# Performance work log

Hardware: AMD Instinct MI355X
Metric: run time of the kernel (lower is better)

Reference implementation:

```python
import jax, jax.numpy as jnp
import numpy as np


def setup_inputs() -> dict:
    key = jax.random.key(0)
    B, S, D = 64, 1024, 1024
    ks = jax.random.split(key, 13)
    bound = 1.0 / np.sqrt(D)
    u = lambda k, shape: jax.random.uniform(k, shape, jnp.float32, -bound, bound)
    inp = {
        "emb": jax.random.normal(ks[0], (B, S, D), jnp.float32),
        "W_ii": u(ks[1], (D, D)), "b_ii": u(ks[2], (D,)),
        "W_if": u(ks[3], (D, D)), "b_if": u(ks[4], (D,)),
        "W_ig": u(ks[5], (D, D)), "b_ig": u(ks[6], (D,)),
        "W_io": u(ks[7], (D, D)), "b_io": u(ks[8], (D,)),
        "W_hi": u(ks[9], (D, D)),
        "W_hf": u(ks[10], (D, D)),
        "W_hg": u(ks[11], (D, D)),
        "W_ho": u(ks[12], (D, D)),
    }
    return inp


def _lstm_forward(emb, W_ii, b_ii, W_if, b_if, W_ig, b_ig, W_io, b_io,
                  W_hi, W_hf, W_hg, W_ho):
    B, S, D = emb.shape
    # Precompute all input projections in one batched GEMM: [B,S,4D]
    Wx = jnp.concatenate([W_ii, W_if, W_ig, W_io], axis=0)      # [4D, D]
    bx = jnp.concatenate([b_ii, b_if, b_ig, b_io], axis=0)      # [4D]
    x_proj = jnp.einsum('bsd,ed->bse', emb, Wx) + bx            # [B,S,4D]
    x_proj = jnp.swapaxes(x_proj, 0, 1)                         # [S,B,4D]
    # Fuse the 4 hidden matmuls into one [D,4D] weight
    Wh = jnp.concatenate([W_hi, W_hf, W_hg, W_ho], axis=0)      # [4D, D]

    h0 = jnp.zeros((B, D), emb.dtype)
    c0 = jnp.zeros((B, D), emb.dtype)

    def step(carry, xp_t):
        h, c = carry
        gates = xp_t + h @ Wh.T                                 # [B,4D]
        xi, xf, xg, xo = jnp.split(gates, 4, axis=-1)
        i_t = jax.nn.sigmoid(xi)
        f_t = jax.nn.sigmoid(xf)
        g_t = jnp.tanh(xg)
        o_t = jax.nn.sigmoid(xo)
        c = f_t * c + i_t * g_t
        h = o_t * jnp.tanh(c)
        return (h, c), None

    (h, c), _ = jax.lax.scan(step, (h0, c0), x_proj)
    return h


def reference(emb, W_ii, b_ii, W_if, b_if, W_ig, b_ig, W_io, b_io,
              W_hi, W_hf, W_hg, W_ho):
    return _lstm_forward(emb, W_ii, b_ii, W_if, b_if, W_ig, b_ig,
                         W_io, b_io, W_hi, W_hf, W_hg, W_ho)
```

## Files before the change

### kernel.cpp

```cpp
#include <hip/hip_runtime.h>
#include <stdint.h>

#define NB 64
#define NS 1024
#define ND 1024
#define NG 4096
#define CHUNK 128
#define NCHUNK 8
#define RING 32

typedef __attribute__((ext_vector_type(4))) float f32x4;
typedef __attribute__((ext_vector_type(8))) short bf16x8;

__device__ __forceinline__ float bf2f(uint16_t u) {
  return __uint_as_float(((uint32_t)u) << 16);
}
__device__ __forceinline__ uint16_t f2bf(float f) {
  uint32_t x = __float_as_uint(f);
  return (uint16_t)((x + 0x7fffu + ((x >> 16) & 1u)) >> 16);
}
__device__ __forceinline__ float sigmoidf_(float x) {
  return 1.f / (1.f + __expf(-x));
}
__device__ __forceinline__ float tanhf_(float x) {
  return 1.f - 2.f / (__expf(x + x) + 1.f);
}
__device__ __forceinline__ void gload_lds16(const void* g, void* l) {
  __builtin_amdgcn_global_load_lds(
      (const __attribute__((address_space(1))) uint32_t*)g,
      (__attribute__((address_space(3))) uint32_t*)l, 16, 0, 0);
}
__device__ __forceinline__ void gload_lds16_nc(const void* g, void* l) {
  __builtin_amdgcn_global_load_lds(
      (const __attribute__((address_space(1))) uint32_t*)g,
      (__attribute__((address_space(3))) uint32_t*)l, 16, 0, 17);
}

__global__ void k_cvt(const float* __restrict__ src, uint16_t* __restrict__ dst, int n4) {
  int stride = gridDim.x * blockDim.x;
  for (int i = blockIdx.x * blockDim.x + threadIdx.x; i < n4; i += stride) {
    float4 v = ((const float4*)src)[i];
    ushort4 o;
    o.x = f2bf(v.x); o.y = f2bf(v.y); o.z = f2bf(v.z); o.w = f2bf(v.w);
    ((ushort4*)dst)[i] = o;
  }
}

__device__ __forceinline__ void gemm_tile(const uint16_t* __restrict__ A0,
                                          const uint16_t* __restrict__ Wx,
                                          uint16_t* __restrict__ XP,
                                          int b, int nb, int tid, char* lmem) {
  uint16_t* lAx = (uint16_t*)lmem;
  uint16_t* lBx = (uint16_t*)(lmem + 8192);
  const uint16_t* B0 = Wx + (size_t)(nb * 128) * ND;
  const int lane = tid & 63, wv = tid >> 6;
  const int m_off = (wv >> 1) << 6, n_off = (wv & 1) << 6;

  f32x4 acc[4][4] = {};
  for (int kb = 0; kb < ND / 32; ++kb) {
    const int k0 = kb * 32;
#pragma unroll
    for (int j = 0; j < 2; ++j) {
      int cid = j * 256 + tid;
      int row = cid >> 2, cc = cid & 3;
      int cs = cc ^ (row & 3);
      gload_lds16(A0 + (size_t)row * ND + k0 + cs * 8, (char*)lAx + cid * 16);
      gload_lds16(B0 + (size_t)row * ND + k0 + cs * 8, (char*)lBx + cid * 16);
    }
    __syncthreads();
    bf16x8 af[4], bfr[4];
#pragma unroll
    for (int i = 0; i < 4; ++i) {
      int row = m_off + i * 16 + (lane & 15);
      int ch = (lane >> 4) ^ (row & 3);
      af[i] = *(const bf16x8*)((const char*)lAx + row * 64 + ch * 16);
      int rowb = n_off + i * 16 + (lane & 15);
      int chb = (lane >> 4) ^ (rowb & 3);
      bfr[i] = *(const bf16x8*)((const char*)lBx + rowb * 64 + chb * 16);
    }
#pragma unroll
    for (int i = 0; i < 4; ++i)
#pragma unroll
      for (int j2 = 0; j2 < 4; ++j2)
        acc[i][j2] = __builtin_amdgcn_mfma_f32_16x16x32_bf16(af[i], bfr[j2], acc[i][j2], 0, 0, 0);
    __syncthreads();
  }
#pragma unroll
  for (int i = 0; i < 4; ++i)
#pragma unroll
    for (int j2 = 0; j2 < 4; ++j2)
#pragma unroll
      for (int r = 0; r < 4; ++r) {
        int m = m_off + i * 16 + ((lane >> 4) << 2) + r;
        int n = nb * 128 + n_off + j2 * 16 + (lane & 15);
        XP[((size_t)(m * NB + b)) * NG + n] = f2bf(acc[i][j2][r]);
      }
}

__global__ __launch_bounds__(512, 2) void k_fused(
    const uint16_t* __restrict__ embb,
    const uint16_t* __restrict__ Wx,
    const uint16_t* __restrict__ Wh,
    uint16_t* __restrict__ xpA, uint16_t* __restrict__ xpB,
    const float* __restrict__ b_i, const float* __restrict__ b_f,
    const float* __restrict__ b_g, const float* __restrict__ b_o,
    uint16_t* __restrict__ hring,
    float* __restrict__ cbuf,
    uint32_t* __restrict__ flags,
    float* __restrict__ out, int chunk) {
  extern __shared__ char smem[];
  const int bid = blockIdx.x;
  const int tid = threadIdx.x;

  if (chunk < 0 || bid >= 128) {
    const int gc = (chunk < 0) ? 0 : chunk + 1;
    if (gc >= NCHUNK) return;
    uint16_t* XP = (gc & 1) ? xpB : xpA;
    const int nw = (chunk < 0) ? 512 : 256;
    const int widx = ((chunk < 0) ? bid : bid - 128) * 2 + (tid >> 8);
    const int t256 = tid & 255;
    char* lmem = smem + ((tid >> 8) << 14);
    const int t0g = gc * CHUNK;
    for (int job = widx; job < 64 * 32; job += nw) {
      int b = job & 63, nb = job >> 6;
      gemm_tile(embb + ((size_t)b * NS + t0g) * ND, Wx, XP, b, nb, t256, lmem);
    }
    return;
  }

  uint16_t* lH = (uint16_t*)smem;
  int* lds_sync = (int*)(smem + 32768);
  const int t0 = chunk * CHUNK;
  const uint16_t* XP = (chunk & 1) ? xpB : xpA;

  const int lane = tid & 63, wv = tid >> 6;
  const int xcd = bid & 7;
  const int g_b = xcd >> 1;
  const int g_d = (xcd & 1) + ((bid >> 3) << 1);

  const int q = lane >> 4, nl = lane & 15;
  const int g = nl & 3;
  const int d_loc = wv * 4 + (nl >> 2);
  const int dg = g_d * 32 + d_loc;
  const int bg0 = g_b * 16 + q * 4;

  const uint16_t* wrow = Wh + ((size_t)g * ND + dg) * ND;
  bf16x8 wfr[32];
#pragma unroll
  for (int kk = 0; kk < 32; ++kk)
    wfr[kk] = *(const bf16x8*)(wrow + kk * 32 + q * 8);

  const float* bptr = (g == 0) ? b_i : (g == 1) ? b_f : (g == 2) ? b_g : b_o;
  const float Bv = bptr[dg];

  float c0, c1, c2, c3;
  if (t0 == 0) {
    c0 = c1 = c2 = c3 = 0.f;
  } else {
    c0 = cbuf[(size_t)(bg0 + 0) * ND + dg];
    c1 = cbuf[(size_t)(bg0 + 1) * ND + dg];
    c2 = cbuf[(size_t)(bg0 + 2) * ND + dg];
    c3 = cbuf[(size_t)(bg0 + 3) * ND + dg];
  }

  if (tid == 0)
    __hip_atomic_store(lds_sync, t0, __ATOMIC_RELAXED, __HIP_MEMORY_SCOPE_WORKGROUP);
  __syncthreads();

  const uint16_t* xp0 = XP + ((size_t)bg0) * NG + ((size_t)g << 10) + dg;
  uint16_t xc0 = xp0[0], xc1 = xp0[NG], xc2 = xp0[2 * (size_t)NG], xc3 = xp0[3 * (size_t)NG];

#pragma unroll 1
  for (int t = t0; t < t0 + CHUNK; ++t) {
    f32x4 a0 = {0,0,0,0}, a1 = {0,0,0,0}, a2 = {0,0,0,0}, a3 = {0,0,0,0};
    if (t > 0) {
      if (wv == 0) {
        const uint32_t* fl = flags + ((((size_t)(t - 1) * 4 + g_b) << 5) + (lane & 31)) * 4;
        uint32_t v;
        do {
          v = __hip_atomic_load(fl, __ATOMIC_RELAXED, __HIP_MEMORY_SCOPE_AGENT);
        } while (__any(v == 0));
        if (lane == 0)
          __hip_atomic_store(lds_sync, t, __ATOMIC_RELAXED, __HIP_MEMORY_SCOPE_WORKGROUP);
      } else {
        while (__hip_atomic_load(lds_sync, __ATOMIC_RELAXED, __HIP_MEMORY_SCOPE_WORKGROUP) < t) {}
      }
      const uint16_t* hbase = hring + (size_t)((t - 1) & (RING - 1)) * NB * ND;
#pragma unroll
      for (int j = 0; j < 4; ++j) {
        int ch = wv * 64 + j * 512 + lane;
        int row = ch >> 7, c = ch & 127;
        const uint16_t* src = hbase + (size_t)(g_b * 16 + row) * ND + ((c ^ (row & 7)) << 3);
        gload_lds16_nc(src, (char*)lH + ch * 16);
      }
      __syncthreads();
    }

    int tn = t + 1 < t0 + CHUNK ? t + 1 : t;
    const uint16_t* xpn = XP + (((size_t)(tn - t0) * NB) + bg0) * NG + ((size_t)g << 10) + dg;
    uint16_t xn0 = xpn[0], xn1 = xpn[NG], xn2 = xpn[2 * (size_t)NG], xn3 = xpn[3 * (size_t)NG];

    if (t > 0) {
#pragma unroll
      for (int kk = 0; kk < 32; ++kk) {
        int cs = (kk * 4 + q) ^ (nl & 7);
        bf16x8 af = *(const bf16x8*)((const char*)lH + nl * 2048 + cs * 16);
        if ((kk & 3) == 0)      a0 = __builtin_amdgcn_mfma_f32_16x16x32_bf16(af, wfr[kk], a0, 0, 0, 0);
        else if ((kk & 3) == 1) a1 = __builtin_amdgcn_mfma_f32_16x16x32_bf16(af, wfr[kk], a1, 0, 0, 0);
        else if ((kk & 3) == 2) a2 = __builtin_amdgcn_mfma_f32_16x16x32_bf16(af, wfr[kk], a2, 0, 0, 0);
        else                    a3 = __builtin_amdgcn_mfma_f32_16x16x32_bf16(af, wfr[kk], a3, 0, 0, 0);
      }
    }

    float xr[4] = { bf2f(xc0), bf2f(xc1), bf2f(xc2), bf2f(xc3) };
    float cc[4] = { c0, c1, c2, c3 };
    float hval = 0.f;
#pragma unroll
    for (int r = 0; r < 4; ++r) {
      float v = a0[r] + a1[r] + a2[r] + a3[r] + xr[r] + Bv;
      float act = (g == 2) ? tanhf_(v) : sigmoidf_(v);
      float s1 = __shfl_xor(act, 1);
      float pe = (g & 1) ? s1 : act;
      float po = (g & 1) ? act : s1;
      float qe = __shfl_xor(pe, 2);
      float qo = __shfl_xor(po, 2);
      float gi = (g & 2) ? qe : pe;
      float gf = (g & 2) ? qo : po;
      float gg2 = (g & 2) ? pe : qe;
      float go = (g & 2) ? po : qo;
      float cn = __builtin_fmaf(gf, cc[r], gi * gg2);
      cc[r] = cn;
      float h = go * tanhf_(cn);
      if (r == g) hval = h;
    }
    c0 = cc[0]; c1 = cc[1]; c2 = cc[2]; c3 = cc[3];

    {
      int hv = (int)f2bf(hval);
      int p = __shfl_xor(hv, 4);
      uint32_t v32 = ((nl >> 2) & 1) ? ((uint32_t)p | ((uint32_t)hv << 16))
                                     : ((uint32_t)hv | ((uint32_t)p << 16));
      uint32_t hi = (uint32_t)__shfl_xor((int)v32, 8);
      if (nl < 4) {
        uint64_t val = (uint64_t)v32 | ((uint64_t)hi << 32);
        uint16_t* dst = hring + (size_t)(t & (RING - 1)) * NB * ND
                        + (size_t)(g_b * 16 + q * 4 + nl) * ND + g_d * 32 + wv * 4;
        __hip_atomic_store((uint64_t*)dst, val, __ATOMIC_RELAXED, __HIP_MEMORY_SCOPE_AGENT);
      }
    }
    if (t == NS - 1) out[(size_t)(bg0 + g) * ND + dg] = hval;

    __syncthreads();
    if (tid == 0)
      __hip_atomic_store(flags + ((((size_t)t * 4 + g_b) << 5) + g_d) * 4, 1u,
                         __ATOMIC_RELAXED, __HIP_MEMORY_SCOPE_AGENT);

    xc0 = xn0; xc1 = xn1; xc2 = xn2; xc3 = xn3;
  }

  float cstore = (g == 0) ? c0 : (g == 1) ? c1 : (g == 2) ? c2 : c3;
  cbuf[(size_t)(bg0 + g) * ND + dg] = cstore;
}

extern "C" void kernel_launch(void* const* d_in, const int* in_sizes, int n_in,
                              void* d_out, int out_size, void* d_ws, size_t ws_size,
                              hipStream_t stream) {
  const float* emb = (const float*)d_in[0];
  const float* W_ii = (const float*)d_in[1];
  const float* b_ii = (const float*)d_in[2];
  const float* W_if = (const float*)d_in[3];
  const float* b_if = (const float*)d_in[4];
  const float* W_ig = (const float*)d_in[5];
  const float* b_ig = (const float*)d_in[6];
  const float* W_io = (const float*)d_in[7];
  const float* b_io = (const float*)d_in[8];
  const float* W_hi = (const float*)d_in[9];
  const float* W_hf = (const float*)d_in[10];
  const float* W_hg = (const float*)d_in[11];
  const float* W_ho = (const float*)d_in[12];

  char* ws = (char*)d_ws;
  uint16_t* embb  = (uint16_t*)ws;
  uint16_t* wx    = (uint16_t*)(ws + 134217728);
  uint16_t* wh    = (uint16_t*)(ws + 142606336);
  uint16_t* xpA   = (uint16_t*)(ws + 150994944);
  uint16_t* xpB   = (uint16_t*)(ws + 218103808);
  uint16_t* hring = (uint16_t*)(ws + 285212672);
  float*    cbuf  = (float*)(ws + 289406976);
  uint32_t* flags = (uint32_t*)(ws + 289669120);

  hipMemsetAsync(flags, 0, 2097152, stream);

  k_cvt<<<2048, 256, 0, stream>>>(emb, embb, 64 * 1024 * 1024 / 4);
  k_cvt<<<256, 256, 0, stream>>>(W_ii, wx + 0 * 1048576, 262144);
  k_cvt<<<256, 256, 0, stream>>>(W_if, wx + 1 * 1048576, 262144);
  k_cvt<<<256, 256, 0, stream>>>(W_ig, wx + 2 * 1048576, 262144);
  k_cvt<<<256, 256, 0, stream>>>(W_io, wx + 3 * 1048576, 262144);
  k_cvt<<<256, 256, 0, stream>>>(W_hi, wh + 0 * 1048576, 262144);
  k_cvt<<<256, 256, 0, stream>>>(W_hf, wh + 1 * 1048576, 262144);
  k_cvt<<<256, 256, 0, stream>>>(W_hg, wh + 2 * 1048576, 262144);
  k_cvt<<<256, 256, 0, stream>>>(W_ho, wh + 3 * 1048576, 262144);

  const int SHM = 98304;
  hipFuncSetAttribute((const void*)k_fused, hipFuncAttributeMaxDynamicSharedMemorySize, SHM);

  k_fused<<<256, 512, SHM, stream>>>(embb, wx, wh, xpA, xpB, b_ii, b_if, b_ig, b_io,
                                     hring, cbuf, flags, (float*)d_out, -1);
  for (int chk = 0; chk < NCHUNK; ++chk)
    k_fused<<<256, 512, SHM, stream>>>(embb, wx, wh, xpA, xpB, b_ii, b_if, b_ig, b_io,
                                       hring, cbuf, flags, (float*)d_out, chk);
}
```

Before: 3.619 ms.

## Stream per-producer h slices into LDS as flags arrive, using fragment-ordered ring layout

The hidden-state ring is re-laid out so each producer block's 32-column slice is a contiguous 1 KB chunk already in MFMA A-fragment order. The polling wave now issues an LDS load for each slice as soon as that producer's flag is seen, instead of waiting for all 32 flags and then loading the whole tile. This overlaps the h fetch with the barrier wait and replaces the trailing __syncthreads with an LDS progress counter. The projection GEMM tile assignment also becomes fixed 2x2 or 4x2 blocks per wave so consecutive tiles share Wx or emb data. The risk is extra scalar/ballot overhead in the spin loop, and the progress-counter handoff must keep LDS reuse ordering correct.

```diff
diff --git a/kernel.cpp b/kernel.cpp
--- a/kernel.cpp
+++ b/kernel.cpp
@@ -11,6 +11,8 @@
 
 typedef __attribute__((ext_vector_type(4))) float f32x4;
 typedef __attribute__((ext_vector_type(8))) short bf16x8;
+
+#define WAITV0 asm volatile("s_waitcnt vmcnt(0)" ::: "memory")
 
 __device__ __forceinline__ float bf2f(uint16_t u) {
   return __uint_as_float(((uint32_t)u) << 16);
@@ -116,22 +118,38 @@
     const int gc = (chunk < 0) ? 0 : chunk + 1;
     if (gc >= NCHUNK) return;
     uint16_t* XP = (gc & 1) ? xpB : xpA;
-    const int nw = (chunk < 0) ? 512 : 256;
-    const int widx = ((chunk < 0) ? bid : bid - 128) * 2 + (tid >> 8);
+    const int t0g = gc * CHUNK;
     const int t256 = tid & 255;
     char* lmem = smem + ((tid >> 8) << 14);
-    const int t0g = gc * CHUNK;
-    for (int job = widx; job < 64 * 32; job += nw) {
-      int b = job & 63, nb = job >> 6;
-      gemm_tile(embb + ((size_t)b * NS + t0g) * ND, Wx, XP, b, nb, t256, lmem);
+    if (chunk < 0) {
+      int w = bid * 2 + (tid >> 8);
+      int wb = w & 31, wn = w >> 5;
+#pragma unroll
+      for (int nbi = 0; nbi < 2; ++nbi)
+#pragma unroll
+        for (int bi = 0; bi < 2; ++bi) {
+          int b = wb * 2 + bi, nb = wn * 2 + nbi;
+          gemm_tile(embb + ((size_t)b * NS + t0g) * ND, Wx, XP, b, nb, t256, lmem);
+        }
+    } else {
+      int w = (bid - 128) * 2 + (tid >> 8);
+      int wb = w & 15, wn = w >> 4;
+#pragma unroll
+      for (int nbi = 0; nbi < 2; ++nbi)
+#pragma unroll
+        for (int bi = 0; bi < 4; ++bi) {
+          int b = wb * 4 + bi, nb = wn * 2 + nbi;
+          gemm_tile(embb + ((size_t)b * NS + t0g) * ND, Wx, XP, b, nb, t256, lmem);
+        }
     }
     return;
   }
 
-  uint16_t* lH = (uint16_t*)smem;
-  int* lds_sync = (int*)(smem + 32768);
+  char* lbuf = smem;
+  int* prog = (int*)(smem + 32768);
   const int t0 = chunk * CHUNK;
   const uint16_t* XP = (chunk & 1) ? xpB : xpA;
+  const char* hring_b = (const char*)hring;
 
   const int lane = tid & 63, wv = tid >> 6;
   const int xcd = bid & 7;
@@ -143,6 +161,7 @@
   const int d_loc = wv * 4 + (nl >> 2);
   const int dg = g_d * 32 + d_loc;
   const int bg0 = g_b * 16 + q * 4;
+  const int aoff = (nl * 4 + q) * 16;
 
   const uint16_t* wrow = Wh + ((size_t)g * ND + dg) * ND;
   bf16x8 wfr[32];
@@ -164,7 +183,7 @@
   }
 
   if (tid == 0)
-    __hip_atomic_store(lds_sync, t0, __ATOMIC_RELAXED, __HIP_MEMORY_SCOPE_WORKGROUP);
+    __hip_atomic_store(prog, 0, __ATOMIC_RELAXED, __HIP_MEMORY_SCOPE_WORKGROUP);
   __syncthreads();
 
   const uint16_t* xp0 = XP + ((size_t)bg0) * NG + ((size_t)g << 10) + dg;
@@ -172,39 +191,37 @@
 
 #pragma unroll 1
   for (int t = t0; t < t0 + CHUNK; ++t) {
-    f32x4 a0 = {0,0,0,0}, a1 = {0,0,0,0}, a2 = {0,0,0,0}, a3 = {0,0,0,0};
-    if (t > 0) {
-      if (wv == 0) {
-        const uint32_t* fl = flags + ((((size_t)(t - 1) * 4 + g_b) << 5) + (lane & 31)) * 4;
-        uint32_t v;
-        do {
-          v = __hip_atomic_load(fl, __ATOMIC_RELAXED, __HIP_MEMORY_SCOPE_AGENT);
-        } while (__any(v == 0));
-        if (lane == 0)
-          __hip_atomic_store(lds_sync, t, __ATOMIC_RELAXED, __HIP_MEMORY_SCOPE_WORKGROUP);
-      } else {
-        while (__hip_atomic_load(lds_sync, __ATOMIC_RELAXED, __HIP_MEMORY_SCOPE_WORKGROUP) < t) {}
-      }
-      const uint16_t* hbase = hring + (size_t)((t - 1) & (RING - 1)) * NB * ND;
-#pragma unroll
-      for (int j = 0; j < 4; ++j) {
-        int ch = wv * 64 + j * 512 + lane;
-        int row = ch >> 7, c = ch & 127;
-        const uint16_t* src = hbase + (size_t)(g_b * 16 + row) * ND + ((c ^ (row & 7)) << 3);
-        gload_lds16_nc(src, (char*)lH + ch * 16);
-      }
-      __syncthreads();
-    }
-
     int tn = t + 1 < t0 + CHUNK ? t + 1 : t;
     const uint16_t* xpn = XP + (((size_t)(tn - t0) * NB) + bg0) * NG + ((size_t)g << 10) + dg;
     uint16_t xn0 = xpn[0], xn1 = xpn[NG], xn2 = xpn[2 * (size_t)NG], xn3 = xpn[3 * (size_t)NG];
 
+    f32x4 a0 = {0,0,0,0}, a1 = {0,0,0,0}, a2 = {0,0,0,0}, a3 = {0,0,0,0};
     if (t > 0) {
+      const int sstep = (chunk == 0) ? (t - 1) : (t - t0);
+      if (wv == 0) {
+        const char* hb = hring_b + (size_t)((t - 1) & (RING - 1)) * 131072
+                       + (size_t)g_b * 32768;
+        const uint32_t* fl = flags + ((((size_t)(t - 1) * 4 + g_b) << 5) + (lane & 31)) * 4;
+        uint64_t got = 0;
+        while (got != 0xffffffffull) {
+          uint32_t v = (lane < 32)
+              ? __hip_atomic_load(fl, __ATOMIC_RELAXED, __HIP_MEMORY_SCOPE_AGENT) : 1u;
+          uint64_t avail = (__ballot(v != 0) & 0xffffffffull) & ~got;
+          while (avail) {
+            int p = __builtin_ctzll(avail); avail &= avail - 1;
+            gload_lds16_nc(hb + p * 1024 + lane * 16, lbuf + p * 1024 + lane * 16);
+            got |= 1ull << p;
+          }
+        }
+        WAITV0;
+        __hip_atomic_store(prog, sstep + 1, __ATOMIC_RELAXED, __HIP_MEMORY_SCOPE_WORKGROUP);
+      } else {
+        while (__hip_atomic_load(prog, __ATOMIC_RELAXED, __HIP_MEMORY_SCOPE_WORKGROUP)
+               < sstep + 1) {}
+      }
 #pragma unroll
       for (int kk = 0; kk < 32; ++kk) {
-        int cs = (kk * 4 + q) ^ (nl & 7);
-        bf16x8 af = *(const bf16x8*)((const char*)lH + nl * 2048 + cs * 16);
+        bf16x8 af = *(const bf16x8*)(lbuf + kk * 1024 + aoff);
         if ((kk & 3) == 0)      a0 = __builtin_amdgcn_mfma_f32_16x16x32_bf16(af, wfr[kk], a0, 0, 0, 0);
         else if ((kk & 3) == 1) a1 = __builtin_amdgcn_mfma_f32_16x16x32_bf16(af, wfr[kk], a1, 0, 0, 0);
         else if ((kk & 3) == 2) a2 = __builtin_amdgcn_mfma_f32_16x16x32_bf16(af, wfr[kk], a2, 0, 0, 0);
@@ -243,8 +260,9 @@
       uint32_t hi = (uint32_t)__shfl_xor((int)v32, 8);
       if (nl < 4) {
         uint64_t val = (uint64_t)v32 | ((uint64_t)hi << 32);
-        uint16_t* dst = hring + (size_t)(t & (RING - 1)) * NB * ND
-                        + (size_t)(g_b * 16 + q * 4 + nl) * ND + g_d * 32 + wv * 4;
+        char* dst = (char*)hring + (size_t)(t & (RING - 1)) * 131072
+                  + (size_t)g_b * 32768 + (size_t)g_d * 1024
+                  + ((q * 4 + nl) * 4 + (wv >> 1)) * 16 + (wv & 1) * 8;
         __hip_atomic_store((uint64_t*)dst, val, __ATOMIC_RELAXED, __HIP_MEMORY_SCOPE_AGENT);
       }
     }
```

Measured after the change: 4.638 ms. +28.2%, slower.

## Assign recurrent roles by hardware XCC id and fuse weight conversions

Applied to the files above, without the earlier changes.

Each workgroup reads its XCC id from a hardware register and claims a slot with an atomic counter. Roles follow the physical die: XCCs 0-3 run the recurrence for one batch group each, and XCCs 4-7 run the next chunk's input-projection GEMM, tiled so each wave reuses one batch row across several weight tiles. The hidden-state ring is now loaded with an L2-cached hint instead of non-temporal, and the eight weight conversion launches become one kernel. The aim is to keep the h exchange and flag polling inside a die's L2 and to cut launch overhead. The cost is relying on the hardware dispatching exactly 32 blocks per XCC; if that does not hold, slots overflow and the mapping breaks.

```diff
diff --git a/kernel.cpp b/kernel.cpp
--- a/kernel.cpp
+++ b/kernel.cpp
@@ -30,15 +30,37 @@
       (const __attribute__((address_space(1))) uint32_t*)g,
       (__attribute__((address_space(3))) uint32_t*)l, 16, 0, 0);
 }
-__device__ __forceinline__ void gload_lds16_nc(const void* g, void* l) {
+__device__ __forceinline__ void gload_lds16_l2(const void* g, void* l) {
   __builtin_amdgcn_global_load_lds(
       (const __attribute__((address_space(1))) uint32_t*)g,
-      (__attribute__((address_space(3))) uint32_t*)l, 16, 0, 17);
+      (__attribute__((address_space(3))) uint32_t*)l, 16, 0, 1);
 }
 
 __global__ void k_cvt(const float* __restrict__ src, uint16_t* __restrict__ dst, int n4) {
   int stride = gridDim.x * blockDim.x;
   for (int i = blockIdx.x * blockDim.x + threadIdx.x; i < n4; i += stride) {
+    float4 v = ((const float4*)src)[i];
+    ushort4 o;
+    o.x = f2bf(v.x); o.y = f2bf(v.y); o.z = f2bf(v.z); o.w = f2bf(v.w);
+    ((ushort4*)dst)[i] = o;
+  }
+}
+
+__global__ void k_cvt8(const float* w0, const float* w1, const float* w2, const float* w3,
+                       const float* w4, const float* w5, const float* w6, const float* w7,
+                       uint16_t* wx, uint16_t* wh) {
+  int which = blockIdx.x >> 8;
+  const float* src;
+  uint16_t* dst;
+  if      (which == 0) { src = w0; dst = wx; }
+  else if (which == 1) { src = w1; dst = wx + 1048576; }
+  else if (which == 2) { src = w2; dst = wx + 2097152; }
+  else if (which == 3) { src = w3; dst = wx + 3145728; }
+  else if (which == 4) { src = w4; dst = wh; }
+  else if (which == 5) { src = w5; dst = wh + 1048576; }
+  else if (which == 6) { src = w6; dst = wh + 2097152; }
+  else                 { src = w7; dst = wh + 3145728; }
+  for (int i = (blockIdx.x & 255) * 256 + threadIdx.x; i < 262144; i += 65536) {
     float4 v = ((const float4*)src)[i];
     ushort4 o;
     o.x = f2bf(v.x); o.y = f2bf(v.y); o.z = f2bf(v.z); o.w = f2bf(v.w);
@@ -107,23 +129,51 @@
     uint16_t* __restrict__ hring,
     float* __restrict__ cbuf,
     uint32_t* __restrict__ flags,
+    uint32_t* __restrict__ claim,
     float* __restrict__ out, int chunk) {
   extern __shared__ char smem[];
   const int bid = blockIdx.x;
   const int tid = threadIdx.x;
 
-  if (chunk < 0 || bid >= 128) {
+  int xcc = 0, slot = 0;
+  if (chunk >= 0) {
+    __shared__ int s_role;
+    if (tid == 0) {
+      int x = (int)(__builtin_amdgcn_s_getreg((31 << 11) | 20)) & 7;
+      int s = (int)atomicAdd(&claim[(chunk + 1) * 8 + x], 1u);
+      s_role = (x << 8) | s;
+    }
+    __syncthreads();
+    int rv = s_role;
+    xcc = rv >> 8; slot = rv & 255;
+  }
+
+  if (chunk < 0 || xcc >= 4) {
     const int gc = (chunk < 0) ? 0 : chunk + 1;
     if (gc >= NCHUNK) return;
     uint16_t* XP = (gc & 1) ? xpB : xpA;
-    const int nw = (chunk < 0) ? 512 : 256;
-    const int widx = ((chunk < 0) ? bid : bid - 128) * 2 + (tid >> 8);
     const int t256 = tid & 255;
     char* lmem = smem + ((tid >> 8) << 14);
     const int t0g = gc * CHUNK;
-    for (int job = widx; job < 64 * 32; job += nw) {
-      int b = job & 63, nb = job >> 6;
-      gemm_tile(embb + ((size_t)b * NS + t0g) * ND, Wx, XP, b, nb, t256, lmem);
+    if (chunk < 0) {
+      int w = bid * 2 + (tid >> 8);
+      int wb = w & 31, wn = w >> 5;
+#pragma unroll
+      for (int nbi = 0; nbi < 2; ++nbi)
+#pragma unroll
+        for (int bi = 0; bi < 2; ++bi) {
+          int b = wb * 2 + bi, nb = wn * 2 + nbi;
+          gemm_tile(embb + ((size_t)b * NS + t0g) * ND, Wx, XP, b, nb, t256, lmem);
+        }
+    } else {
+      int xp2 = xcc - 4;
+      int u = slot * 2 + (tid >> 8);
+      int b = xp2 * 16 + (u & 15);
+      int nb0 = u >> 4;
+      const uint16_t* A0 = embb + ((size_t)b * NS + t0g) * ND;
+#pragma unroll
+      for (int k2 = 0; k2 < 8; ++k2)
+        gemm_tile(A0, Wx, XP, b, nb0 + 4 * k2, t256, lmem);
     }
     return;
   }
@@ -134,9 +184,8 @@
   const uint16_t* XP = (chunk & 1) ? xpB : xpA;
 
   const int lane = tid & 63, wv = tid >> 6;
-  const int xcd = bid & 7;
-  const int g_b = xcd >> 1;
-  const int g_d = (xcd & 1) + ((bid >> 3) << 1);
+  const int g_b = xcc;
+  const int g_d = slot;
 
   const int q = lane >> 4, nl = lane & 15;
   const int g = nl & 3;
@@ -191,7 +240,7 @@
         int ch = wv * 64 + j * 512 + lane;
         int row = ch >> 7, c = ch & 127;
         const uint16_t* src = hbase + (size_t)(g_b * 16 + row) * ND + ((c ^ (row & 7)) << 3);
-        gload_lds16_nc(src, (char*)lH + ch * 16);
+        gload_lds16_l2(src, (char*)lH + ch * 16);
       }
       __syncthreads();
     }
@@ -288,25 +337,19 @@
   uint16_t* hring = (uint16_t*)(ws + 285212672);
   float*    cbuf  = (float*)(ws + 289406976);
   uint32_t* flags = (uint32_t*)(ws + 289669120);
-
-  hipMemsetAsync(flags, 0, 2097152, stream);
+  uint32_t* claim = (uint32_t*)(ws + 291766272);
+
+  hipMemsetAsync(flags, 0, 2097152 + 512, stream);
 
   k_cvt<<<2048, 256, 0, stream>>>(emb, embb, 64 * 1024 * 1024 / 4);
-  k_cvt<<<256, 256, 0, stream>>>(W_ii, wx + 0 * 1048576, 262144);
-  k_cvt<<<256, 256, 0, stream>>>(W_if, wx + 1 * 1048576, 262144);
-  k_cvt<<<256, 256, 0, stream>>>(W_ig, wx + 2 * 1048576, 262144);
-  k_cvt<<<256, 256, 0, stream>>>(W_io, wx + 3 * 1048576, 262144);
-  k_cvt<<<256, 256, 0, stream>>>(W_hi, wh + 0 * 1048576, 262144);
-  k_cvt<<<256, 256, 0, stream>>>(W_hf, wh + 1 * 1048576, 262144);
-  k_cvt<<<256, 256, 0, stream>>>(W_hg, wh + 2 * 1048576, 262144);
-  k_cvt<<<256, 256, 0, stream>>>(W_ho, wh + 3 * 1048576, 262144);
+  k_cvt8<<<2048, 256, 0, stream>>>(W_ii, W_if, W_ig, W_io, W_hi, W_hf, W_hg, W_ho, wx, wh);
 
   const int SHM = 98304;
   hipFuncSetAttribute((const void*)k_fused, hipFuncAttributeMaxDynamicSharedMemorySize, SHM);
 
   k_fused<<<256, 512, SHM, stream>>>(embb, wx, wh, xpA, xpB, b_ii, b_if, b_ig, b_io,
-                                     hring, cbuf, flags, (float*)d_out, -1);
+                                     hring, cbuf, flags, claim, (float*)d_out, -1);
   for (int chk = 0; chk < NCHUNK; ++chk)
     k_fused<<<256, 512, SHM, stream>>>(embb, wx, wh, xpA, xpB, b_ii, b_if, b_ig, b_io,
-                                       hring, cbuf, flags, (float*)d_out, chk);
-}
+                                       hring, cbuf, flags, claim, (float*)d_out, chk);
+}
```

Measured after the change: 9.890 ms. 2.73x slower.
